# Kernel tuning notes

Hardware: AMD Instinct MI355X
Metric: run time of the kernel (lower is better)

Reference implementation:

```python
import jax, jax.numpy as jnp
import numpy as np

V = 32000      # vocab
TMAX = 1024    # BLOCK_SIZE
D = 768        # N_EMBD
H = 12         # N_HEAD
L = 12         # N_LAYER
HS = D // H    # head_size
FF = 4 * D
B, T = 4, 1024


def setup_inputs() -> dict:
    key = jax.random.key(0)
    ks = iter(jax.random.split(key, 40))
    n = lambda shape: 0.02 * jax.random.normal(next(ks), shape, dtype=jnp.float32)
    return dict(
        idx=jax.random.randint(next(ks), (B, T), 0, V),
        targets=jax.random.randint(next(ks), (B, T), 0, V),
        tok_emb=n((V, D)),
        pos_emb=n((TMAX, D)),
        Wq=n((L, H, D, HS)), Wk=n((L, H, D, HS)), Wv=n((L, H, D, HS)),
        Wo=n((L, D, D)), bo=jnp.zeros((L, D)),
        W1=n((L, D, FF)), b1=jnp.zeros((L, FF)),
        W2=n((L, FF, D)), b2=jnp.zeros((L, D)),
        ln1_g=jnp.ones((L, D)), ln1_b=jnp.zeros((L, D)),
        ln2_g=jnp.ones((L, D)), ln2_b=jnp.zeros((L, D)),
        lnf_g=jnp.ones((D,)), lnf_b=jnp.zeros((D,)),
        Wlm=n((D, V)), blm=jnp.zeros((V,)),
    )


def _ln(x, g, b, eps=1e-5):
    m = x.mean(-1, keepdims=True)
    v = x.var(-1, keepdims=True)
    return (x - m) * jax.lax.rsqrt(v + eps) * g + b


def reference(idx, targets, tok_emb, pos_emb, Wq, Wk, Wv, Wo, bo,
              W1, b1, W2, b2, ln1_g, ln1_b, ln2_g, ln2_b, lnf_g, lnf_b,
              Wlm, blm):
    Bsz, Tt = idx.shape
    x = tok_emb[idx] + pos_emb[:Tt]                      # [B,T,D]
    causal = jnp.tril(jnp.ones((Tt, Tt), dtype=bool))     # [T,T]

    def layer(x, p):
        wq, wk, wv, wo, bob, w1, b1b, w2, b2b, g1, be1, g2, be2 = p
        h = _ln(x, g1, be1)
        q = jnp.einsum('btd,hdk->bhtk', h, wq)
        k = jnp.einsum('btd,hdk->bhtk', h, wk)
        v = jnp.einsum('btd,hdk->bhtk', h, wv)
        wei = jnp.einsum('bhtk,bhsk->bhts', q, k) * (HS ** -0.5)
        wei = jnp.where(causal, wei, -jnp.inf)
        wei = jax.nn.softmax(wei, axis=-1)                # dropout=0 in eval
        att = jnp.einsum('bhts,bhsk->bhtk', wei, v)
        att = att.transpose(0, 2, 1, 3).reshape(Bsz, Tt, H * HS)  # concat heads
        x = x + att @ wo + bob
        h2 = _ln(x, g2, be2)
        x = x + jax.nn.relu(h2 @ w1 + b1b) @ w2 + b2b
        return x, None

    x, _ = jax.lax.scan(layer, x,
                        (Wq, Wk, Wv, Wo, bo, W1, b1, W2, b2,
                         ln1_g, ln1_b, ln2_g, ln2_b))
    x = _ln(x, lnf_g, lnf_b)
    logits = x @ Wlm + blm                                # [B,T,V]
    lf = logits.reshape(Bsz * Tt, V)
    tf = targets.reshape(-1)
    logp = jax.nn.log_softmax(lf, axis=-1)
    loss = -jnp.take_along_axis(logp, tf[:, None], axis=1).mean()
    return lf, loss
```

## Files before the change

### kernel.cpp

```cpp
#include <hip/hip_runtime.h>

constexpr int C_B   = 4;
constexpr int C_T   = 1024;
constexpr int C_D   = 768;
constexpr int C_H   = 12;
constexpr int C_HS  = 64;
constexpr int C_FF  = 3072;
constexpr int C_V   = 32000;
constexpr int C_L   = 12;
constexpr int ROWS  = C_B * C_T;
constexpr int QKVN  = 3 * C_D;

typedef __bf16 bf16;
typedef __attribute__((ext_vector_type(8))) __bf16 bf16x8;
typedef __attribute__((ext_vector_type(4))) float  f32x4;
typedef __attribute__((ext_vector_type(4))) short  s16x4;

static __device__ __forceinline__ void gload16(const void* g, void* l) {
  __builtin_amdgcn_global_load_lds((const __attribute__((address_space(1))) void*)g,
                                   (__attribute__((address_space(3))) void*)l,
                                   16, 0, 0);
}

__global__ __launch_bounds__(256) void embed_kernel(const int* __restrict__ idx,
    const float* __restrict__ tok, const float* __restrict__ pos, float* __restrict__ x) {
  int gid = blockIdx.x * 256 + threadIdx.x;
  int row = gid / C_D, d = gid - row * C_D;
  int t = row & (C_T - 1);
  x[gid] = tok[(long)idx[row] * C_D + d] + pos[(long)t * C_D + d];
}

__global__ __launch_bounds__(256) void ln_kernel(const float* __restrict__ x,
    const float* __restrict__ g, const float* __restrict__ bb, long goff,
    bf16* __restrict__ out) {
  int row = blockIdx.x, tid = threadIdx.x;
  const float* xr = x + (long)row * C_D;
  float v0 = xr[tid], v1 = xr[tid + 256], v2 = xr[tid + 512];
  float s = v0 + v1 + v2;
  float s2 = v0 * v0 + v1 * v1 + v2 * v2;
#pragma unroll
  for (int off = 32; off > 0; off >>= 1) {
    s  += __shfl_down(s, off);
    s2 += __shfl_down(s2, off);
  }
  __shared__ float sm[4], sq[4];
  if ((tid & 63) == 0) { sm[tid >> 6] = s; sq[tid >> 6] = s2; }
  __syncthreads();
  s  = sm[0] + sm[1] + sm[2] + sm[3];
  s2 = sq[0] + sq[1] + sq[2] + sq[3];
  float mean = s * (1.f / C_D);
  float var  = s2 * (1.f / C_D) - mean * mean;
  float rstd = rsqrtf(var + 1e-5f);
  bf16* orow = out + (long)row * C_D;
  orow[tid]       = (bf16)((v0 - mean) * rstd * g[goff + tid]       + bb[goff + tid]);
  orow[tid + 256] = (bf16)((v1 - mean) * rstd * g[goff + tid + 256] + bb[goff + tid + 256]);
  orow[tid + 512] = (bf16)((v2 - mean) * rstd * g[goff + tid + 512] + bb[goff + tid + 512]);
}

__global__ __launch_bounds__(256) void transpose_kernel(const float* __restrict__ src,
    bf16* __restrict__ dst, int K, int N, long soff0, int ntn) {
  __shared__ bf16 tile[32][33];
  const float* s = src + soff0;
  int tn = blockIdx.x % ntn, tk = blockIdx.x / ntn;
  int c = threadIdx.x & 31, r = threadIdx.x >> 5;
#pragma unroll
  for (int it = 0; it < 4; ++it)
    tile[r + 8 * it][c] = (bf16)s[(long)(tk * 32 + r + 8 * it) * N + tn * 32 + c];
  __syncthreads();
#pragma unroll
  for (int it = 0; it < 4; ++it)
    dst[(long)(tn * 32 + r + 8 * it) * K + tk * 32 + c] = tile[c][r + 8 * it];
}

__global__ __launch_bounds__(256) void transpose_layer_kernel(
    const float* __restrict__ Wq, const float* __restrict__ Wk,
    const float* __restrict__ Wv, const float* __restrict__ Wo,
    const float* __restrict__ W1, const float* __restrict__ W2,
    bf16* __restrict__ wqkvt, bf16* __restrict__ wot,
    bf16* __restrict__ w1t, bf16* __restrict__ w2t, int l) {
  int bid = blockIdx.x;
  const float* src; bf16* dst; int K, N, ntn, t;
  if (bid < 1728) {
    int which = bid / 576, r = bid % 576, head = r / 48;
    t = r % 48;
    const float* W = which == 0 ? Wq : which == 1 ? Wk : Wv;
    src = W + (long)l * C_H * C_D * C_HS + (long)head * C_D * C_HS;
    dst = wqkvt + (long)which * C_D * C_D + (long)head * C_HS * C_D;
    K = C_D; N = C_HS; ntn = 2;
  } else if (bid < 2304) {
    t = bid - 1728; src = Wo + (long)l * C_D * C_D; dst = wot;
    K = C_D; N = C_D; ntn = 24;
  } else if (bid < 4608) {
    t = bid - 2304; src = W1 + (long)l * C_D * C_FF; dst = w1t;
    K = C_D; N = C_FF; ntn = 96;
  } else {
    t = bid - 4608; src = W2 + (long)l * C_FF * C_D; dst = w2t;
    K = C_FF; N = C_D; ntn = 24;
  }
  __shared__ bf16 tile[32][33];
  int tn = t % ntn, tk = t / ntn;
  int c = threadIdx.x & 31, r = threadIdx.x >> 5;
#pragma unroll
  for (int it = 0; it < 4; ++it)
    tile[r + 8 * it][c] = (bf16)src[(long)(tk * 32 + r + 8 * it) * N + tn * 32 + c];
  __syncthreads();
#pragma unroll
  for (int it = 0; it < 4; ++it)
    dst[(long)(tn * 32 + r + 8 * it) * K + tk * 32 + c] = tile[c][r + 8 * it];
}

template <int MODE>
__global__ __launch_bounds__(256) void gemm_bt(const bf16* __restrict__ A,
    const bf16* __restrict__ Bt, const float* __restrict__ bias, long boff,
    void* __restrict__ outp, float* __restrict__ resid, int N, int K) {
  __shared__ __attribute__((aligned(16))) char smem[32768];
  int tid = threadIdx.x;
  int l = tid & 63;
  int w = tid >> 6, wr = w >> 1, wc = w & 1;
  int lg = l >> 4, lr = l & 15;

  int nwg = gridDim.x;
  int fid = blockIdx.x;
  int swz = (fid & 7) * (nwg >> 3) + (fid >> 3);
  long row0 = (long)(swz & 31) * 128;
  long col0 = (long)(swz >> 5) * 128;

  const bf16* ga = A  + (row0 + (tid >> 2)) * K + (tid & 3) * 8;
  const bf16* gb = Bt + (col0 + (tid >> 2)) * K + (tid & 3) * 8;

  f32x4 acc[4][4];
  const f32x4 fz = {0.f, 0.f, 0.f, 0.f};
#pragma unroll
  for (int m = 0; m < 4; ++m)
#pragma unroll
    for (int n = 0; n < 4; ++n) acc[m][n] = fz;

  int nk = K >> 5;
  {
    bf16* la = (bf16*)smem + tid * 8;
    bf16* lb = (bf16*)(smem + 8192) + tid * 8;
    gload16(ga, la);  gload16(ga + (long)64 * K, la + 2048);
    gload16(gb, lb);  gload16(gb + (long)64 * K, lb + 2048);
    ga += 32; gb += 32;
  }
  int cur = 0;
  for (int t = 0; t < nk; ++t) {
    __syncthreads();
    if (t + 1 < nk) {
      char* bufb = smem + (cur ^ 1) * 16384;
      bf16* la = (bf16*)bufb + tid * 8;
      bf16* lb = (bf16*)(bufb + 8192) + tid * 8;
      gload16(ga, la);  gload16(ga + (long)64 * K, la + 2048);
      gload16(gb, lb);  gload16(gb + (long)64 * K, lb + 2048);
      ga += 32; gb += 32;
    }
    const bf16* cA = (const bf16*)(smem + cur * 16384);
    const bf16* cB = (const bf16*)(smem + cur * 16384 + 8192);
    bf16x8 af[4], bfr[4];
#pragma unroll
    for (int m = 0; m < 4; ++m)
      af[m] = *(const bf16x8*)(cA + (wr * 64 + m * 16 + lr) * 32 + lg * 8);
#pragma unroll
    for (int n = 0; n < 4; ++n)
      bfr[n] = *(const bf16x8*)(cB + (wc * 64 + n * 16 + lr) * 32 + lg * 8);
#pragma unroll
    for (int m = 0; m < 4; ++m)
#pragma unroll
      for (int n = 0; n < 4; ++n)
        acc[m][n] = __builtin_amdgcn_mfma_f32_16x16x32_bf16(af[m], bfr[n], acc[m][n], 0, 0, 0);
    cur ^= 1;
  }
  __syncthreads();

  if (MODE == 0 || MODE == 1) {
    bf16* lc = (bf16*)smem;
#pragma unroll
    for (int n = 0; n < 4; ++n) {
      int gcl = wc * 64 + n * 16 + lr;
      float bv = bias ? bias[boff + col0 + gcl] : 0.f;
#pragma unroll
      for (int m = 0; m < 4; ++m) {
        int rb = wr * 64 + m * 16 + lg * 4;
#pragma unroll
        for (int r = 0; r < 4; ++r) {
          float v = acc[m][n][r] + bv;
          if (MODE == 1) v = fmaxf(v, 0.f);
          lc[(rb + r) * 128 + gcl] = (bf16)v;
        }
      }
    }
    __syncthreads();
#pragma unroll
    for (int it = 0; it < 8; ++it) {
      int byte = it * 4096 + tid * 16;
      int rl = byte >> 8;
      int cb = byte & 255;
      bf16x8 v = *(const bf16x8*)(smem + byte);
      *(bf16x8*)((bf16*)outp + (row0 + rl) * N + col0 + (cb >> 1)) = v;
    }
  } else {
#pragma unroll
    for (int pair = 0; pair < 2; ++pair) {
      float* lcf = (float*)smem;
#pragma unroll
      for (int n = 0; n < 4; ++n) {
        int gcl = wc * 64 + n * 16 + lr;
        float bv = bias ? bias[boff + col0 + gcl] : 0.f;
#pragma unroll
        for (int mi = 0; mi < 2; ++mi) {
          int m = pair * 2 + mi;
          int rl = wr * 32 + mi * 16 + lg * 4;
#pragma unroll
          for (int r = 0; r < 4; ++r)
            lcf[(rl + r) * 128 + gcl] = acc[m][n][r] + bv;
        }
      }
      __syncthreads();
#pragma unroll
      for (int it = 0; it < 8; ++it) {
        int byte = it * 4096 + tid * 16;
        int rl = byte >> 9;
        int cb = byte & 511;
        long gr = row0 + (rl >> 5) * 64 + pair * 32 + ((rl >> 4) & 1) * 16 + (rl & 15);
        f32x4 v = *(const f32x4*)(smem + byte);
        if (MODE == 2) {
          f32x4 g = *(const f32x4*)(resid + gr * N + col0 + (cb >> 2));
          v += g;
          *(f32x4*)(resid + gr * N + col0 + (cb >> 2)) = v;
        } else {
          *(f32x4*)((float*)outp + gr * N + col0 + (cb >> 2)) = v;
        }
      }
      __syncthreads();
    }
  }
}

#define TRRD(D, OFF) asm volatile("ds_read_b64_tr_b16 %0, %1 offset:" OFF \
                                  : "=v"(D) : "v"(trp))
__global__ __launch_bounds__(64) void attn_kernel(const bf16* __restrict__ qkv,
                                                  bf16* __restrict__ attout) {
  int fid = blockIdx.x;
  int swzb = (fid & 7) * 384 + (fid >> 3);
  int qt = swzb & 63;
  int bh = swzb >> 6;
  int b = bh / C_H, h = bh % C_H;
  int l = threadIdx.x;
  int lg = l >> 4, lr = l & 15;
  const bf16* base = qkv + (long)b * C_T * QKVN;

  const bf16* qp = base + (long)(qt * 16 + lr) * QKVN + h * C_HS;
  bf16x8 qf0 = *(const bf16x8*)(qp + lg * 8);
  bf16x8 qf1 = *(const bf16x8*)(qp + 32 + lg * 8);

  const f32x4 fz = {0.f, 0.f, 0.f, 0.f};
  f32x4 o[4] = {fz, fz, fz, fz};
  float m_run[4], l_run[4];
#pragma unroll
  for (int r = 0; r < 4; ++r) { m_run[r] = -1e30f; l_run[r] = 0.f; }

  __shared__ __attribute__((aligned(16))) bf16 p_lds[16][40];
  __shared__ __attribute__((aligned(16))) bf16 vt_sub[2048];

  unsigned trp = (unsigned)(unsigned long)
      ((const __attribute__((address_space(3))) char*)vt_sub + l * 8);

  int nkt = (qt * 16 + 15) / 32 + 1;
  for (int kt = 0; kt < nkt; ++kt) {
    int key0 = kt * 32;
    f32x4 sacc[2];
#pragma unroll
    for (int ss = 0; ss < 2; ++ss) {
      const bf16* kp = base + (long)(key0 + ss * 16 + lr) * QKVN + C_D + h * C_HS;
      bf16x8 kf0 = *(const bf16x8*)(kp + lg * 8);
      bf16x8 kf1 = *(const bf16x8*)(kp + 32 + lg * 8);
      f32x4 a = fz;
      a = __builtin_amdgcn_mfma_f32_16x16x32_bf16(qf0, kf0, a, 0, 0, 0);
      a = __builtin_amdgcn_mfma_f32_16x16x32_bf16(qf1, kf1, a, 0, 0, 0);
      sacc[ss] = a;
    }
#pragma unroll
    for (int r = 0; r < 4; ++r) {
      int qrow = qt * 16 + lg * 4 + r;
      bool u0 = (key0 + lr) <= qrow;
      bool u1 = (key0 + 16 + lr) <= qrow;
      float s0 = u0 ? sacc[0][r] * 0.125f : -1e30f;
      float s1 = u1 ? sacc[1][r] * 0.125f : -1e30f;
      float mr = fmaxf(s0, s1);
      mr = fmaxf(mr, __shfl_xor(mr, 1));
      mr = fmaxf(mr, __shfl_xor(mr, 2));
      mr = fmaxf(mr, __shfl_xor(mr, 4));
      mr = fmaxf(mr, __shfl_xor(mr, 8));
      float mnew = fmaxf(m_run[r], mr);
      float scale = __expf(m_run[r] - mnew);
      float p0 = u0 ? __expf(s0 - mnew) : 0.f;
      float p1 = u1 ? __expf(s1 - mnew) : 0.f;
      float rs = p0 + p1;
      rs += __shfl_xor(rs, 1);
      rs += __shfl_xor(rs, 2);
      rs += __shfl_xor(rs, 4);
      rs += __shfl_xor(rs, 8);
      l_run[r] = l_run[r] * scale + rs;
      m_run[r] = mnew;
      o[0][r] *= scale; o[1][r] *= scale; o[2][r] *= scale; o[3][r] *= scale;
      p_lds[lg * 4 + r][lr]      = (bf16)p0;
      p_lds[lg * 4 + r][16 + lr] = (bf16)p1;
    }
#pragma unroll
    for (int it = 0; it < 4; ++it) {
      int kl = it * 8 + (l >> 3);
      int d0 = (l & 7) * 8;
      bf16x8 vv = *(const bf16x8*)(base + (long)(key0 + kl) * QKVN + 2 * C_D + h * C_HS + d0);
      int ba = ((d0 >> 4) << 10) + (((kl >> 2) & 1) << 9) + ((kl >> 3) << 7)
             + ((kl & 3) << 5) + ((d0 & 15) << 1);
      *(bf16x8*)((char*)vt_sub + ba) = vv;
    }
    __syncthreads();
    s16x4 t0a, t0b, t1a, t1b, t2a, t2b, t3a, t3b;
    TRRD(t0a, "0");    TRRD(t0b, "512");
    TRRD(t1a, "1024"); TRRD(t1b, "1536");
    TRRD(t2a, "2048"); TRRD(t2b, "2560");
    TRRD(t3a, "3072"); TRRD(t3b, "3584");
    bf16x8 pf = *(const bf16x8*)(&p_lds[lr][lg * 8]);
    asm volatile("s_waitcnt lgkmcnt(0)" ::: "memory");
    __builtin_amdgcn_sched_barrier(0);
    union uu { short s[8]; bf16x8 v; };
    auto mk = [](s16x4 a, s16x4 bq) {
      uu u;
      u.s[0] = a[0]; u.s[1] = a[1]; u.s[2] = a[2]; u.s[3] = a[3];
      u.s[4] = bq[0]; u.s[5] = bq[1]; u.s[6] = bq[2]; u.s[7] = bq[3];
      return u.v;
    };
    o[0] = __builtin_amdgcn_mfma_f32_16x16x32_bf16(pf, mk(t0a, t0b), o[0], 0, 0, 0);
    o[1] = __builtin_amdgcn_mfma_f32_16x16x32_bf16(pf, mk(t1a, t1b), o[1], 0, 0, 0);
    o[2] = __builtin_amdgcn_mfma_f32_16x16x32_bf16(pf, mk(t2a, t2b), o[2], 0, 0, 0);
    o[3] = __builtin_amdgcn_mfma_f32_16x16x32_bf16(pf, mk(t3a, t3b), o[3], 0, 0, 0);
    __syncthreads();
  }
#pragma unroll
  for (int c = 0; c < 4; ++c)
#pragma unroll
    for (int r = 0; r < 4; ++r) {
      int qrow = qt * 16 + lg * 4 + r;
      attout[((long)b * C_T + qrow) * C_D + h * C_HS + c * 16 + lr] =
          (bf16)(o[c][r] / l_run[r]);
    }
}

__global__ __launch_bounds__(256) void loss_kernel(const float* __restrict__ logits,
    const int* __restrict__ targets, float* __restrict__ rowloss) {
  int row = blockIdx.x, tid = threadIdx.x;
  const float* lrow = logits + (long)row * C_V;
  float m = -1e30f, sum = 0.f;
  for (int i4 = tid * 4; i4 < C_V; i4 += 1024) {
    f32x4 v4 = *(const f32x4*)(lrow + i4);
#pragma unroll
    for (int j = 0; j < 4; ++j) {
      float v = v4[j];
      if (v > m) { sum *= __expf(m - v); m = v; }
      sum += __expf(v - m);
    }
  }
#pragma unroll
  for (int off = 32; off > 0; off >>= 1) {
    float mo = __shfl_down(m, off), so = __shfl_down(sum, off);
    float M = fmaxf(m, mo);
    sum = sum * __expf(m - M) + so * __expf(mo - M);
    m = M;
  }
  __shared__ float sm[4], ss[4];
  if ((tid & 63) == 0) { sm[tid >> 6] = m; ss[tid >> 6] = sum; }
  __syncthreads();
  if (tid == 0) {
    float M = sm[0], S = ss[0];
    for (int wv = 1; wv < 4; ++wv) {
      float M2 = fmaxf(M, sm[wv]);
      S = S * __expf(M - M2) + ss[wv] * __expf(sm[wv] - M2);
      M = M2;
    }
    float lt = lrow[targets[row]];
    rowloss[row] = -(lt - M - logf(S));
  }
}

__global__ __launch_bounds__(256) void loss_final(const float* __restrict__ rowloss,
                                                  float* __restrict__ out) {
  int tid = threadIdx.x;
  float s = 0.f;
  for (int i = tid; i < ROWS; i += 256) s += rowloss[i];
#pragma unroll
  for (int off = 32; off > 0; off >>= 1) s += __shfl_down(s, off);
  __shared__ float sm[4];
  if ((tid & 63) == 0) sm[tid >> 6] = s;
  __syncthreads();
  if (tid == 0) out[0] = (sm[0] + sm[1] + sm[2] + sm[3]) * (1.f / ROWS);
}

extern "C" void kernel_launch(void* const* d_in, const int* in_sizes, int n_in,
                              void* d_out, int out_size, void* d_ws, size_t ws_size,
                              hipStream_t stream) {
  (void)in_sizes; (void)n_in; (void)out_size; (void)ws_size;
  const int*   idx     = (const int*)  d_in[0];
  const int*   targets = (const int*)  d_in[1];
  const float* tok     = (const float*)d_in[2];
  const float* pos     = (const float*)d_in[3];
  const float* Wq      = (const float*)d_in[4];
  const float* Wk      = (const float*)d_in[5];
  const float* Wv      = (const float*)d_in[6];
  const float* Wo      = (const float*)d_in[7];
  const float* bo      = (const float*)d_in[8];
  const float* W1      = (const float*)d_in[9];
  const float* b1      = (const float*)d_in[10];
  const float* W2      = (const float*)d_in[11];
  const float* b2      = (const float*)d_in[12];
  const float* ln1g    = (const float*)d_in[13];
  const float* ln1b    = (const float*)d_in[14];
  const float* ln2g    = (const float*)d_in[15];
  const float* ln2b    = (const float*)d_in[16];
  const float* lnfg    = (const float*)d_in[17];
  const float* lnfb    = (const float*)d_in[18];
  const float* Wlm     = (const float*)d_in[19];
  const float* blm     = (const float*)d_in[20];

  char* p = (char*)d_ws;
  auto alloc = [&](size_t bytes) {
    char* r = p; p += (bytes + 255) & ~(size_t)255; return r;
  };
  float* x       = (float*)alloc((size_t)ROWS * C_D * 4);
  bf16*  h       = (bf16*) alloc((size_t)ROWS * C_D * 2);
  bf16*  qkv     = (bf16*) alloc((size_t)ROWS * QKVN * 2);
  bf16*  attout  = (bf16*) alloc((size_t)ROWS * C_D * 2);
  bf16*  ffbuf   = (bf16*) alloc((size_t)ROWS * C_FF * 2);
  bf16*  wqkvt   = (bf16*) alloc((size_t)QKVN * C_D * 2);
  bf16*  wot     = (bf16*) alloc((size_t)C_D * C_D * 2);
  bf16*  w1t     = (bf16*) alloc((size_t)C_FF * C_D * 2);
  bf16*  w2t     = (bf16*) alloc((size_t)C_D * C_FF * 2);
  float* rowloss = (float*)alloc((size_t)ROWS * 4);
  bf16*  wlmt    = qkv;

  float* logits = (float*)d_out;

  embed_kernel<<<ROWS * C_D / 256, 256, 0, stream>>>(idx, tok, pos, x);

  for (int l = 0; l < C_L; ++l) {
    transpose_layer_kernel<<<6912, 256, 0, stream>>>(
        Wq, Wk, Wv, Wo, W1, W2, wqkvt, wot, w1t, w2t, l);

    ln_kernel<<<ROWS, 256, 0, stream>>>(x, ln1g, ln1b, (long)l * C_D, h);
    gemm_bt<0><<<(QKVN / 128) * 32, 256, 0, stream>>>(
        h, wqkvt, nullptr, 0, qkv, nullptr, QKVN, C_D);
    attn_kernel<<<C_B * C_H * (C_T / 16), 64, 0, stream>>>(qkv, attout);
    gemm_bt<2><<<(C_D / 128) * 32, 256, 0, stream>>>(
        attout, wot, bo, (long)l * C_D, nullptr, x, C_D, C_D);
    ln_kernel<<<ROWS, 256, 0, stream>>>(x, ln2g, ln2b, (long)l * C_D, h);
    gemm_bt<1><<<(C_FF / 128) * 32, 256, 0, stream>>>(
        h, w1t, b1, (long)l * C_FF, ffbuf, nullptr, C_FF, C_D);
    gemm_bt<2><<<(C_D / 128) * 32, 256, 0, stream>>>(
        ffbuf, w2t, b2, (long)l * C_D, nullptr, x, C_D, C_FF);
  }

  transpose_kernel<<<(C_V / 32) * (C_D / 32), 256, 0, stream>>>(
      Wlm, wlmt, C_D, C_V, 0, C_V / 32);

  ln_kernel<<<ROWS, 256, 0, stream>>>(x, lnfg, lnfb, 0, h);
  gemm_bt<3><<<(C_V / 128) * 32, 256, 0, stream>>>(
      h, wlmt, blm, 0, logits, nullptr, C_V, C_D);
  loss_kernel<<<ROWS, 256, 0, stream>>>(logits, targets, rowloss);
  loss_final<<<1, 256, 0, stream>>>(rowloss, logits + (long)ROWS * C_V);
}
```

Baseline: 3.079 ms.

## Add 256x256-tile 512-thread GEMM for QKV, FF1 and LM-head projections

```diff
diff --git a/kernel.cpp b/kernel.cpp
--- a/kernel.cpp
+++ b/kernel.cpp
@@ -110,6 +110,149 @@
 }
 
 template <int MODE>
+__global__ __launch_bounds__(512) void gemm256(const bf16* __restrict__ A,
+    const bf16* __restrict__ Bt, const float* __restrict__ bias, long boff,
+    void* __restrict__ outp, int N, int K) {
+  __shared__ __attribute__((aligned(16))) char smem[131072];
+  int tid = threadIdx.x;
+  int l = tid & 63, w = tid >> 6;
+  int wm = w >> 2, wn = w & 3;
+  int lg = l >> 4, lr = l & 15;
+
+  int nwg = gridDim.x;
+  int fid = blockIdx.x;
+  int swz = (fid & 7) * (nwg >> 3) + (fid >> 3);
+  long row0 = (long)(swz & 15) * 256;
+  long col0 = (long)(swz >> 4) * 256;
+
+  int Y0 = tid * 16, Y1 = 8192 + tid * 16;
+  auto dec = [](int Y, int& R, int& C) {
+    int s = Y >> 10, y = Y & 1023;
+    int r15 = y >> 6, z = y & 63;
+    int q = (z ^ ((r15 & 8) << 2)) >> 4;
+    R = (s >> 1) * 16 + r15;
+    C = (s & 1) * 32 + q * 8;
+  };
+  int R0, C0, R1, C1;
+  dec(Y0, R0, C0);  dec(Y1, R1, C1);
+  const bf16* Ab = A  + row0 * K;
+  const bf16* Bb = Bt + col0 * K;
+
+  auto stage = [&](int d, int kt) {
+    char* bb = smem + d * 65536;
+    long kc = (long)kt * 64;
+    gload16(Ab + (long)R0 * K + kc + C0, bb + Y0);
+    gload16(Ab + (long)R1 * K + kc + C1, bb + Y1);
+    gload16(Ab + (long)(128 + R0) * K + kc + C0, bb + 16384 + Y0);
+    gload16(Ab + (long)(128 + R1) * K + kc + C1, bb + 16384 + Y1);
+    gload16(Bb + (long)R0 * K + kc + C0, bb + 32768 + Y0);
+    gload16(Bb + (long)R1 * K + kc + C1, bb + 32768 + Y1);
+    gload16(Bb + (long)(128 + R0) * K + kc + C0, bb + 49152 + Y0);
+    gload16(Bb + (long)(128 + R1) * K + kc + C1, bb + 49152 + Y1);
+  };
+
+  f32x4 acc[8][4];
+  const f32x4 fz = {0.f, 0.f, 0.f, 0.f};
+#pragma unroll
+  for (int mf = 0; mf < 8; ++mf)
+#pragma unroll
+    for (int nf = 0; nf < 4; ++nf) acc[mf][nf] = fz;
+
+  int aoff = lr * 64 + ((lg * 16) ^ ((lr & 8) << 2));
+  int nk = K >> 6;
+  stage(0, 0);
+  int d = 0;
+  for (int kt = 0; kt < nk; ++kt) {
+    __syncthreads();
+    if (kt + 1 < nk) stage(d ^ 1, kt + 1);
+    const char* aB = smem + d * 65536 + wm * 16384;
+    const char* bB = smem + d * 65536 + 32768 + (wn >> 1) * 16384;
+    bf16x8 bfrag[4][2];
+#pragma unroll
+    for (int nf = 0; nf < 4; ++nf)
+#pragma unroll
+      for (int k = 0; k < 2; ++k)
+        bfrag[nf][k] = *(const bf16x8*)(bB + ((((wn & 1) * 4 + nf) * 2 + k) << 10) + aoff);
+#pragma unroll
+    for (int p = 0; p < 4; ++p) {
+      bf16x8 af[2][2];
+#pragma unroll
+      for (int mi = 0; mi < 2; ++mi)
+#pragma unroll
+        for (int k = 0; k < 2; ++k)
+          af[mi][k] = *(const bf16x8*)(aB + (((p * 2 + mi) * 2 + k) << 10) + aoff);
+      __builtin_amdgcn_s_setprio(1);
+#pragma unroll
+      for (int mi = 0; mi < 2; ++mi)
+#pragma unroll
+        for (int nf = 0; nf < 4; ++nf)
+#pragma unroll
+          for (int k = 0; k < 2; ++k)
+            acc[p * 2 + mi][nf] = __builtin_amdgcn_mfma_f32_16x16x32_bf16(
+                af[mi][k], bfrag[nf][k], acc[p * 2 + mi][nf], 0, 0, 0);
+      __builtin_amdgcn_s_setprio(0);
+    }
+    d ^= 1;
+  }
+  __syncthreads();
+
+  if (MODE == 0 || MODE == 1) {
+    bf16* lc = (bf16*)smem;
+#pragma unroll
+    for (int nf = 0; nf < 4; ++nf) {
+      int col = wn * 64 + nf * 16 + lr;
+      float bv = bias ? bias[boff + col0 + col] : 0.f;
+#pragma unroll
+      for (int mf = 0; mf < 8; ++mf) {
+        int rb = wm * 128 + mf * 16 + lg * 4;
+#pragma unroll
+        for (int r = 0; r < 4; ++r) {
+          float v = acc[mf][nf][r] + bv;
+          if (MODE == 1) v = fmaxf(v, 0.f);
+          lc[(rb + r) * 256 + col] = (bf16)v;
+        }
+      }
+    }
+    __syncthreads();
+#pragma unroll
+    for (int it = 0; it < 16; ++it) {
+      int byte = it * 8192 + tid * 16;
+      int rl = byte >> 9, cb = byte & 511;
+      *(bf16x8*)((bf16*)outp + (row0 + rl) * N + col0 + (cb >> 1)) =
+          *(const bf16x8*)(smem + byte);
+    }
+  } else {
+#pragma unroll
+    for (int h = 0; h < 2; ++h) {
+      if (h) __syncthreads();
+      if (wm == h) {
+        float* lf = (float*)smem;
+#pragma unroll
+        for (int nf = 0; nf < 4; ++nf) {
+          int col = wn * 64 + nf * 16 + lr;
+          float bv = bias ? bias[boff + col0 + col] : 0.f;
+#pragma unroll
+          for (int mf = 0; mf < 8; ++mf) {
+            int rb = mf * 16 + lg * 4;
+#pragma unroll
+            for (int r = 0; r < 4; ++r)
+              lf[(rb + r) * 256 + col] = acc[mf][nf][r] + bv;
+          }
+        }
+      }
+      __syncthreads();
+#pragma unroll
+      for (int it = 0; it < 16; ++it) {
+        int byte = it * 8192 + tid * 16;
+        int rl = byte >> 10, cb = byte & 1023;
+        *(f32x4*)((float*)outp + (row0 + h * 128 + rl) * N + col0 + (cb >> 2)) =
+            *(const f32x4*)(smem + byte);
+      }
+    }
+  }
+}
+
+template <int MODE>
 __global__ __launch_bounds__(256) void gemm_bt(const bf16* __restrict__ A,
     const bf16* __restrict__ Bt, const float* __restrict__ bias, long boff,
     void* __restrict__ outp, float* __restrict__ resid, int N, int K) {
@@ -172,67 +315,39 @@
   }
   __syncthreads();
 
-  if (MODE == 0 || MODE == 1) {
-    bf16* lc = (bf16*)smem;
+#pragma unroll
+  for (int pair = 0; pair < 2; ++pair) {
+    float* lcf = (float*)smem;
 #pragma unroll
     for (int n = 0; n < 4; ++n) {
       int gcl = wc * 64 + n * 16 + lr;
       float bv = bias ? bias[boff + col0 + gcl] : 0.f;
 #pragma unroll
-      for (int m = 0; m < 4; ++m) {
-        int rb = wr * 64 + m * 16 + lg * 4;
-#pragma unroll
-        for (int r = 0; r < 4; ++r) {
-          float v = acc[m][n][r] + bv;
-          if (MODE == 1) v = fmaxf(v, 0.f);
-          lc[(rb + r) * 128 + gcl] = (bf16)v;
-        }
+      for (int mi = 0; mi < 2; ++mi) {
+        int m = pair * 2 + mi;
+        int rl = wr * 32 + mi * 16 + lg * 4;
+#pragma unroll
+        for (int r = 0; r < 4; ++r)
+          lcf[(rl + r) * 128 + gcl] = acc[m][n][r] + bv;
       }
     }
     __syncthreads();
 #pragma unroll
     for (int it = 0; it < 8; ++it) {
       int byte = it * 4096 + tid * 16;
-      int rl = byte >> 8;
-      int cb = byte & 255;
-      bf16x8 v = *(const bf16x8*)(smem + byte);
-      *(bf16x8*)((bf16*)outp + (row0 + rl) * N + col0 + (cb >> 1)) = v;
-    }
-  } else {
-#pragma unroll
-    for (int pair = 0; pair < 2; ++pair) {
-      float* lcf = (float*)smem;
-#pragma unroll
-      for (int n = 0; n < 4; ++n) {
-        int gcl = wc * 64 + n * 16 + lr;
-        float bv = bias ? bias[boff + col0 + gcl] : 0.f;
-#pragma unroll
-        for (int mi = 0; mi < 2; ++mi) {
-          int m = pair * 2 + mi;
-          int rl = wr * 32 + mi * 16 + lg * 4;
-#pragma unroll
-          for (int r = 0; r < 4; ++r)
-            lcf[(rl + r) * 128 + gcl] = acc[m][n][r] + bv;
-        }
+      int rl = byte >> 9;
+      int cb = byte & 511;
+      long gr = row0 + (rl >> 5) * 64 + pair * 32 + ((rl >> 4) & 1) * 16 + (rl & 15);
+      f32x4 v = *(const f32x4*)(smem + byte);
+      if (MODE == 2) {
+        f32x4 g = *(const f32x4*)(resid + gr * N + col0 + (cb >> 2));
+        v += g;
+        *(f32x4*)(resid + gr * N + col0 + (cb >> 2)) = v;
+      } else {
+        *(f32x4*)((float*)outp + gr * N + col0 + (cb >> 2)) = v;
       }
-      __syncthreads();
-#pragma unroll
-      for (int it = 0; it < 8; ++it) {
-        int byte = it * 4096 + tid * 16;
-        int rl = byte >> 9;
-        int cb = byte & 511;
-        long gr = row0 + (rl >> 5) * 64 + pair * 32 + ((rl >> 4) & 1) * 16 + (rl & 15);
-        f32x4 v = *(const f32x4*)(smem + byte);
-        if (MODE == 2) {
-          f32x4 g = *(const f32x4*)(resid + gr * N + col0 + (cb >> 2));
-          v += g;
-          *(f32x4*)(resid + gr * N + col0 + (cb >> 2)) = v;
-        } else {
-          *(f32x4*)((float*)outp + gr * N + col0 + (cb >> 2)) = v;
-        }
-      }
-      __syncthreads();
-    }
+    }
+    __syncthreads();
   }
 }
 
@@ -447,14 +562,14 @@
         Wq, Wk, Wv, Wo, W1, W2, wqkvt, wot, w1t, w2t, l);
 
     ln_kernel<<<ROWS, 256, 0, stream>>>(x, ln1g, ln1b, (long)l * C_D, h);
-    gemm_bt<0><<<(QKVN / 128) * 32, 256, 0, stream>>>(
-        h, wqkvt, nullptr, 0, qkv, nullptr, QKVN, C_D);
+    gemm256<0><<<16 * (QKVN / 256), 512, 0, stream>>>(
+        h, wqkvt, nullptr, 0, qkv, QKVN, C_D);
     attn_kernel<<<C_B * C_H * (C_T / 16), 64, 0, stream>>>(qkv, attout);
     gemm_bt<2><<<(C_D / 128) * 32, 256, 0, stream>>>(
         attout, wot, bo, (long)l * C_D, nullptr, x, C_D, C_D);
     ln_kernel<<<ROWS, 256, 0, stream>>>(x, ln2g, ln2b, (long)l * C_D, h);
-    gemm_bt<1><<<(C_FF / 128) * 32, 256, 0, stream>>>(
-        h, w1t, b1, (long)l * C_FF, ffbuf, nullptr, C_FF, C_D);
+    gemm256<1><<<16 * (C_FF / 256), 512, 0, stream>>>(
+        h, w1t, b1, (long)l * C_FF, ffbuf, C_FF, C_D);
     gemm_bt<2><<<(C_D / 128) * 32, 256, 0, stream>>>(
         ffbuf, w2t, b2, (long)l * C_D, nullptr, x, C_D, C_FF);
   }
@@ -463,8 +578,8 @@
       Wlm, wlmt, C_D, C_V, 0, C_V / 32);
 
   ln_kernel<<<ROWS, 256, 0, stream>>>(x, lnfg, lnfb, 0, h);
-  gemm_bt<3><<<(C_V / 128) * 32, 256, 0, stream>>>(
-      h, wlmt, blm, 0, logits, nullptr, C_V, C_D);
+  gemm256<3><<<16 * (C_V / 256), 512, 0, stream>>>(
+      h, wlmt, blm, 0, logits, C_V, C_D);
   loss_kernel<<<ROWS, 256, 0, stream>>>(logits, targets, rowloss);
   loss_final<<<1, 256, 0, stream>>>(rowloss, logits + (long)ROWS * C_V);
 }
```

Measured after the change: 3.071 ms. No clear change (-0.3%).
